# Optimization experiments

Measured on AMD Instinct MI355X. Metric: run time of the kernel, lower is better.

The kernel has to match this reference:

```python
import jax, jax.numpy as jnp
import numpy as np

N = 4096          # num_nodes
E = 65536         # num edges (avg degree 16)
WALK_LENGTH = 16
OUT_DIM = 8


def setup_inputs() -> dict:
    key = jax.random.key(0)
    k1, k2 = jax.random.split(key, 2)
    edge_index = jax.random.randint(k1, (2, E), 0, N, dtype=jnp.int64)
    # nn.Linear(walk_length, out_dim): weight [out_dim, walk_length], bias [out_dim]
    linear_w = (jax.random.normal(k2, (OUT_DIM, WALK_LENGTH), jnp.float32)
                / np.float32(np.sqrt(WALK_LENGTH)))
    linear_b = jnp.zeros((OUT_DIM,), jnp.float32)
    return {"edge_index": edge_index, "num_nodes": N,
            "linear_w": linear_w, "linear_b": linear_b}


def reference(edge_index, num_nodes, linear_w, linear_b):
    row, col = edge_index[0], edge_index[1]
    # out-degree via scatter_add, clamped to >= 1
    deg = jnp.zeros((num_nodes,), jnp.float32).at[row].add(1.0)
    deg = jnp.maximum(deg, 1.0)
    rw_values = 1.0 / deg[row]                              # [E]
    # random-walk transition matrix P[row, col] = 1/deg[row]
    # (.at[].add sums duplicate edges, matching coalesce())
    P = jnp.zeros((num_nodes, num_nodes), jnp.float32).at[row, col].add(rw_values)
    Pt = P.T

    def step(cur, _):
        cur = Pt @ cur                                      # [N, N]
        return cur, jnp.diagonal(cur)                       # k-step return probs

    cur0 = jnp.eye(num_nodes, dtype=jnp.float32)
    _, diags = jax.lax.scan(step, cur0, None, length=WALK_LENGTH)
    rw_diag = diags.T                                       # [N, walk_length]
    return rw_diag @ linear_w.T + linear_b                  # [N, out_dim]
```

## Files before the change

### kernel.cpp

```cpp
#include <hip/hip_runtime.h>
#include <hip/hip_fp16.h>
#include <hip/hip_fp8.h>

#define NNODES 4096
#define LWALK 16
#define ODIM 8

#define FP8_SCALE 256.0f
#define FP8_INV   0.00390625f
#define FP8_INV2  1.52587890625e-05f

typedef unsigned int uint4n __attribute__((ext_vector_type(4)));
typedef float float2n __attribute__((ext_vector_type(2)));

__device__ __forceinline__ void dec8f(unsigned int lo, unsigned int hi, float* f) {
#if __has_builtin(__builtin_amdgcn_cvt_pk_f32_fp8)
    float2n p;
    p = __builtin_amdgcn_cvt_pk_f32_fp8((int)lo, false); f[0] = p.x; f[1] = p.y;
    p = __builtin_amdgcn_cvt_pk_f32_fp8((int)lo, true);  f[2] = p.x; f[3] = p.y;
    p = __builtin_amdgcn_cvt_pk_f32_fp8((int)hi, false); f[4] = p.x; f[5] = p.y;
    p = __builtin_amdgcn_cvt_pk_f32_fp8((int)hi, true);  f[6] = p.x; f[7] = p.y;
#else
    unsigned int w[2] = {lo, hi};
    const unsigned char* b = (const unsigned char*)w;
#pragma unroll
    for (int i = 0; i < 8; ++i) {
        __hip_fp8_e4m3 t; t.__x = b[i]; f[i] = (float)t;
    }
#endif
}

__device__ __forceinline__ void enc8f(const float* a, unsigned int* lo,
                                      unsigned int* hi) {
#if __has_builtin(__builtin_amdgcn_cvt_pk_fp8_f32)
    int l = 0, h = 0;
    l = __builtin_amdgcn_cvt_pk_fp8_f32(a[0], a[1], l, false);
    l = __builtin_amdgcn_cvt_pk_fp8_f32(a[2], a[3], l, true);
    h = __builtin_amdgcn_cvt_pk_fp8_f32(a[4], a[5], h, false);
    h = __builtin_amdgcn_cvt_pk_fp8_f32(a[6], a[7], h, true);
    *lo = (unsigned int)l; *hi = (unsigned int)h;
#else
    unsigned char b[8];
#pragma unroll
    for (int i = 0; i < 8; ++i)
        b[i] = __hip_cvt_float_to_fp8(a[i], __HIP_SATFINITE, __HIP_E4M3);
    unsigned int w[2];
    __builtin_memcpy(w, b, 8);
    *lo = w[0]; *hi = w[1];
#endif
}

__device__ __forceinline__ void dec16f(uint4n w, float* f) {
    dec8f(w.x, w.y, f);
    dec8f(w.z, w.w, f + 8);
}

__device__ __forceinline__ uint4n enc16f(const float* a) {
    uint4n o;
    unsigned int lo, hi;
    enc8f(a, &lo, &hi);     o.x = lo; o.y = hi;
    enc8f(a + 8, &lo, &hi); o.z = lo; o.w = hi;
    return o;
}

__device__ __forceinline__ unsigned char enc1f(float f) {
#if __has_builtin(__builtin_amdgcn_cvt_pk_fp8_f32)
    return (unsigned char)(__builtin_amdgcn_cvt_pk_fp8_f32(f, 0.f, 0, false) & 0xFF);
#else
    return __hip_cvt_float_to_fp8(f, __HIP_SATFINITE, __HIP_E4M3);
#endif
}

__device__ __forceinline__ float decw(unsigned int packed) {
    return __half2float(__ushort_as_half((unsigned short)(packed >> 16)));
}

__global__ void detect_fmt_k(const void* ei, int E, int* flag) {
    if (blockIdx.x == 0 && threadIdx.x == 0) {
        const long long* p = (const long long*)ei;
        int ok = 1;
        for (int i = 0; i < 64; ++i) {
            long long v = p[i];
            if (v < 0 || v >= NNODES) { ok = 0; break; }
        }
        *flag = ok;
    }
}

__device__ __forceinline__ int load_idx(const void* p, int i, int fmt) {
    if (fmt) return (int)((const long long*)p)[i];
    return ((const int*)p)[i];
}

__global__ void build_deg_cnt_k(const void* ei, int E, int* deg, int* cnt,
                                const int* fmt) {
    int e = blockIdx.x * blockDim.x + threadIdx.x;
    if (e >= E) return;
    int f = *fmt;
    int r = load_idx(ei, e, f);
    int c = load_idx(ei, E + e, f);
    atomicAdd(&deg[r], 1);
    atomicAdd(&cnt[c], 1);
}

__global__ void scan_k(const int* __restrict__ cnt, int* __restrict__ rowptr,
                       int* __restrict__ cursor) {
    __shared__ int sm[1024];
    int tid = threadIdx.x;
    int v0 = (cnt[4 * tid + 0] + 3) & ~3;
    int v1 = (cnt[4 * tid + 1] + 3) & ~3;
    int v2 = (cnt[4 * tid + 2] + 3) & ~3;
    int v3 = (cnt[4 * tid + 3] + 3) & ~3;
    int tsum = v0 + v1 + v2 + v3;
    sm[tid] = tsum;
    __syncthreads();
    int val = tsum;
    for (int off = 1; off < 1024; off <<= 1) {
        int t = (tid >= off) ? sm[tid - off] : 0;
        __syncthreads();
        val += t;
        sm[tid] = val;
        __syncthreads();
    }
    int excl = val - tsum;
    int p0 = excl, p1 = excl + v0, p2 = p1 + v1, p3 = p2 + v2;
    rowptr[4 * tid + 0] = p0; rowptr[4 * tid + 1] = p1;
    rowptr[4 * tid + 2] = p2; rowptr[4 * tid + 3] = p3;
    cursor[4 * tid + 0] = p0; cursor[4 * tid + 1] = p1;
    cursor[4 * tid + 2] = p2; cursor[4 * tid + 3] = p3;
    if (tid == 1023) rowptr[4096] = val;
}

__global__ void fill_pad_k(const void* ei, int E, const int* __restrict__ deg,
                           int* cursor, int* ocursor,
                           unsigned int* __restrict__ ep4,
                           unsigned int* __restrict__ oidx, const int* fmt) {
    int e = blockIdx.x * blockDim.x + threadIdx.x;
    if (e < E) {
        int f = *fmt;
        int r = load_idx(ei, e, f);
        int c = load_idx(ei, E + e, f);
        int d = deg[r];
        float v = 1.0f / (float)(d < 1 ? 1 : d);
        int pos = atomicAdd(&cursor[c], 1);
        unsigned hv = (unsigned)__half_as_ushort(__float2half(v));
        ep4[pos] = (hv << 16) | (unsigned)r;
        int opos = atomicAdd(&ocursor[r], 1);
        oidx[opos] = (unsigned)c;
    }
}

__global__ void pad_fill_k(const int* __restrict__ rowptr,
                           const int* __restrict__ cursor,
                           unsigned int* __restrict__ ep4) {
    int c = blockIdx.x * blockDim.x + threadIdx.x;
    if (c >= NNODES) return;
    for (int p = cursor[c]; p < rowptr[c + 1]; ++p)
        ep4[p] = 0u;
}

__global__ __launch_bounds__(512, 1) void chain_k(
    const int* __restrict__ rowptr, const unsigned int* __restrict__ ep4,
    const int* __restrict__ orowptr, const int* __restrict__ ocursor,
    const unsigned int* __restrict__ oidx, const int* __restrict__ deg,
    float* __restrict__ rw,
    unsigned char* __restrict__ M4, unsigned char* __restrict__ M5,
    unsigned char* __restrict__ M7, unsigned char* __restrict__ M8) {
    __shared__ unsigned char bufA[NNODES * 16];
    __shared__ unsigned char bufB[NNODES * 16];
    const int t = threadIdx.x;
    const int bid = blockIdx.x;
    const int slab = (bid & 7) * 32 + (bid >> 3);
    const int S0 = slab * 16;

    float* col32 = (float*)bufB;
    const int g = t >> 4;
    const int l = t & 15;
    for (int cl = 0; cl < 16; ++cl) {
        const int gc = S0 + cl;
        for (int i = t; i < NNODES; i += 512) col32[i] = 0.f;
        __syncthreads();
        const int dg = deg[gc];
        const float vg = 1.f / (float)(dg < 1 ? 1 : dg);
        const int ob = orowptr[gc], oe = ocursor[gc];
        for (int p1 = ob + g; p1 < oe; p1 += 32) {
            int m = (int)oidx[p1];
            if (m == gc && l == 0)
                atomicAdd(&rw[gc * LWALK + 0], vg);
            int dm = deg[m];
            float vm = vg / (float)(dm < 1 ? 1 : dm);
            int mb = orowptr[m], me = ocursor[m];
            for (int p2 = mb + l; p2 < me; p2 += 16)
                atomicAdd(&col32[oidx[p2]], vm);
        }
        __syncthreads();
        if (t == 0) rw[gc * LWALK + 1] = col32[gc];
        for (int i = t; i < NNODES; i += 512)
            bufA[i * 16 + cl] = enc1f(col32[i] * FP8_SCALE);
        __syncthreads();
    }

    int rpb[8], rpe[8];
#pragma unroll
    for (int j = 0; j < 8; ++j) {
        rpb[j] = rowptr[t + 512 * j];
        rpe[j] = rowptr[t + 512 * j + 1];
    }
#pragma unroll 1
    for (int k = 3; k <= 8; ++k) {
        const unsigned char* src = (k & 1) ? bufA : bufB;
        unsigned char* dst = (k & 1) ? bufB : bufA;
        __syncthreads();
#pragma unroll 1
        for (int j = 0; j < 8; ++j) {
            const int c = t + 512 * j;
            float acc[16];
#pragma unroll
            for (int u = 0; u < 16; ++u) acc[u] = 0.f;
            for (int e = rpb[j]; e < rpe[j]; e += 4) {
                uint4n ew = *(const uint4n*)(ep4 + e);
                uint4n x0 = *(const uint4n*)(src + (ew.x & 0xFFFFu) * 16);
                uint4n x1 = *(const uint4n*)(src + (ew.y & 0xFFFFu) * 16);
                uint4n x2 = *(const uint4n*)(src + (ew.z & 0xFFFFu) * 16);
                uint4n x3 = *(const uint4n*)(src + (ew.w & 0xFFFFu) * 16);
                float f[16];
                float v;
                v = decw(ew.x);
                dec16f(x0, f);
#pragma unroll
                for (int u = 0; u < 16; ++u) acc[u] = fmaf(f[u], v, acc[u]);
                v = decw(ew.y);
                dec16f(x1, f);
#pragma unroll
                for (int u = 0; u < 16; ++u) acc[u] = fmaf(f[u], v, acc[u]);
                v = decw(ew.z);
                dec16f(x2, f);
#pragma unroll
                for (int u = 0; u < 16; ++u) acc[u] = fmaf(f[u], v, acc[u]);
                v = decw(ew.w);
                dec16f(x3, f);
#pragma unroll
                for (int u = 0; u < 16; ++u) acc[u] = fmaf(f[u], v, acc[u]);
            }
            if ((unsigned)(c - S0) < 16u) {
                float d = 0.f;
#pragma unroll
                for (int u = 0; u < 16; ++u)
                    if (c - S0 == u) d = acc[u];
                rw[c * LWALK + (k - 1)] = d * FP8_INV;
            }
            uint4n o = enc16f(acc);
            *(uint4n*)(dst + c * 16) = o;
        }
        __syncthreads();
        if (k == 4 || k == 5 || k == 7 || k == 8) {
            unsigned char* M = (k == 4) ? M4 : (k == 5) ? M5 : (k == 7) ? M7 : M8;
#pragma unroll 1
            for (int j = 0; j < 8; ++j) {
                const int c = t + 512 * j;
                uint4n o = *(const uint4n*)(dst + c * 16);
                *(uint4n*)(M + (size_t)c * NNODES + S0) = o;
            }
        }
    }
}

__global__ __launch_bounds__(256) void pairall_k(
    const unsigned char* __restrict__ M4, const unsigned char* __restrict__ M5,
    const unsigned char* __restrict__ M7, const unsigned char* __restrict__ M8,
    float* __restrict__ rw) {
    __shared__ __half bt[64][66];
    __shared__ __half ct[64][66];
    const int bid = blockIdx.x;
    const int grp = bid >> 10;
    const int pb = bid & 1023;
    const unsigned char* PA;
    const unsigned char* PB1;
    const unsigned char* PB2;
    int colO, colE;
    if (grp == 0)      { PA = M5; PB1 = M4; PB2 = M5; colO = 8;  colE = 9;  }
    else if (grp == 1) { PA = M7; PB1 = M4; PB2 = M7; colO = 10; colE = 13; }
    else if (grp == 2) { PA = M8; PB1 = M4; PB2 = M8; colO = 11; colE = 15; }
    else               { PA = M8; PB1 = M5; PB2 = M7; colO = 12; colE = 14; }
    const int i0 = (pb & 63) * 64;
    const int Jbeg = (pb >> 6) * (NNODES / 16);
    const int Jend = Jbeg + (NNODES / 16);
    const int t = threadIdx.x;
    const int li = t >> 2;
    const int q = t & 3;
    const int c0 = q * 16;
    float accO = 0.f, accE = 0.f;
    for (int J = Jbeg; J < Jend; J += 64) {
        uint4n b16 = __builtin_nontemporal_load(
            (const uint4n*)(PB1 + (size_t)(J + li) * NNODES + i0 + c0));
        uint4n g16 = __builtin_nontemporal_load(
            (const uint4n*)(PB2 + (size_t)(J + li) * NNODES + i0 + c0));
        __syncthreads();
        float bf[16], gf[16];
        dec16f(b16, bf);
        dec16f(g16, gf);
#pragma unroll
        for (int s = 0; s < 16; ++s) {
            bt[c0 + s][li] = __float2half(bf[s]);
            ct[c0 + s][li] = __float2half(gf[s]);
        }
        __syncthreads();
        uint4n a16 = __builtin_nontemporal_load(
            (const uint4n*)(PA + (size_t)(i0 + li) * NNODES + J + c0));
        float af[16];
        dec16f(a16, af);
#pragma unroll
        for (int s = 0; s < 16; ++s) {
            accO = fmaf(af[s], __half2float(bt[li][c0 + s]), accO);
            accE = fmaf(af[s], __half2float(ct[li][c0 + s]), accE);
        }
    }
    accO += __shfl_xor(accO, 1);
    accO += __shfl_xor(accO, 2);
    accE += __shfl_xor(accE, 1);
    accE += __shfl_xor(accE, 2);
    if (q == 0) {
        atomicAdd(&rw[(i0 + li) * LWALK + colO], accO * FP8_INV2);
        atomicAdd(&rw[(i0 + li) * LWALK + colE], accE * FP8_INV2);
    }
}

__global__ void linear_k(const float* __restrict__ rw, const float* __restrict__ W,
                         const float* __restrict__ b, float* __restrict__ out) {
    int i = blockIdx.x * blockDim.x + threadIdx.x;
    if (i >= NNODES * ODIM) return;
    int s = i >> 3, d = i & 7;
    float acc = b[d];
#pragma unroll
    for (int k = 0; k < LWALK; ++k)
        acc = fmaf(rw[s * LWALK + k], W[d * LWALK + k], acc);
    out[i] = acc;
}

extern "C" void kernel_launch(void* const* d_in, const int* in_sizes, int n_in,
                              void* d_out, int out_size, void* d_ws, size_t ws_size,
                              hipStream_t stream) {
    const void* ei = d_in[0];
    int E = in_sizes[0] / 2;
    const float* W = (const float*)d_in[2];
    const float* bias = (const float*)d_in[3];
    float* out = (float*)d_out;

    char* ws = (char*)d_ws;
    size_t off = 0;
    auto alloc = [&](size_t bytes) -> char* {
        char* p = ws + off;
        off = (off + bytes + 255) & ~(size_t)255;
        return p;
    };
    int* flag = (int*)alloc(4);
    int* deg = (int*)alloc(NNODES * 4);
    int* cnt = (int*)alloc(NNODES * 4);
    int* rowptr = (int*)alloc((NNODES + 1) * 4);
    int* cursor = (int*)alloc(NNODES * 4);
    int* orowptr = (int*)alloc((NNODES + 1) * 4);
    int* ocursor = (int*)alloc(NNODES * 4);
    unsigned int* ep4 = (unsigned int*)alloc(((size_t)E + 4 * NNODES) * 4);
    unsigned int* oidx = (unsigned int*)alloc(((size_t)E + 4 * NNODES) * 4);
    float* rw = (float*)alloc(NNODES * LWALK * 4);
    unsigned char* M4 = (unsigned char*)alloc((size_t)NNODES * NNODES);
    unsigned char* M5 = (unsigned char*)alloc((size_t)NNODES * NNODES);
    unsigned char* M7 = (unsigned char*)alloc((size_t)NNODES * NNODES);
    unsigned char* M8 = (unsigned char*)alloc((size_t)NNODES * NNODES);

    (void)hipMemsetAsync(deg, 0, NNODES * 4, stream);
    (void)hipMemsetAsync(cnt, 0, NNODES * 4, stream);
    (void)hipMemsetAsync(rw, 0, NNODES * LWALK * 4, stream);
    detect_fmt_k<<<1, 64, 0, stream>>>(ei, E, flag);
    build_deg_cnt_k<<<(E + 255) / 256, 256, 0, stream>>>(ei, E, deg, cnt, flag);
    scan_k<<<1, 1024, 0, stream>>>(cnt, rowptr, cursor);
    scan_k<<<1, 1024, 0, stream>>>(deg, orowptr, ocursor);
    fill_pad_k<<<(E + 255) / 256, 256, 0, stream>>>(ei, E, deg, cursor, ocursor,
                                                    ep4, oidx, flag);
    pad_fill_k<<<(NNODES + 255) / 256, 256, 0, stream>>>(rowptr, cursor, ep4);

    chain_k<<<256, 512, 0, stream>>>(rowptr, ep4, orowptr, ocursor, oidx, deg,
                                     rw, M4, M5, M7, M8);

    pairall_k<<<4096, 256, 0, stream>>>(M4, M5, M7, M8, rw);

    linear_k<<<(NNODES * ODIM + 255) / 256, 256, 0, stream>>>(rw, W, bias, out);
}
```

Measured before the change: 357.9 us.

## Halve chain slab width to 8 columns and launch 512 blocks

The propagation kernel now processes 8 identity columns per block instead of 16, using 32 KiB of LDS per 8-column buffer pair instead of 64 KiB. It launches 512 blocks rather than 256, and the launch bound is raised to allow several blocks per CU. This is meant to raise occupancy and fill more CUs on a 256-CU part. In exchange, the edge list and index loads are repeated twice as often per column, with narrower 8-byte LDS gathers.

```diff
diff --git a/kernel.cpp b/kernel.cpp
--- a/kernel.cpp
+++ b/kernel.cpp
@@ -159,24 +159,23 @@
         ep4[p] = 0u;
 }
 
-__global__ __launch_bounds__(512, 1) void chain_k(
+__global__ __launch_bounds__(512, 4) void chain_k(
     const int* __restrict__ rowptr, const unsigned int* __restrict__ ep4,
     const int* __restrict__ orowptr, const int* __restrict__ ocursor,
     const unsigned int* __restrict__ oidx, const int* __restrict__ deg,
     float* __restrict__ rw,
     unsigned char* __restrict__ M4, unsigned char* __restrict__ M5,
     unsigned char* __restrict__ M7, unsigned char* __restrict__ M8) {
-    __shared__ unsigned char bufA[NNODES * 16];
-    __shared__ unsigned char bufB[NNODES * 16];
+    __shared__ unsigned char buf[2][NNODES * 8];
     const int t = threadIdx.x;
     const int bid = blockIdx.x;
-    const int slab = (bid & 7) * 32 + (bid >> 3);
-    const int S0 = slab * 16;
-
-    float* col32 = (float*)bufB;
+    const int slab = (bid & 7) * 64 + (bid >> 3);
+    const int S0 = slab * 8;
+
+    float* col32 = (float*)buf[1];
     const int g = t >> 4;
     const int l = t & 15;
-    for (int cl = 0; cl < 16; ++cl) {
+    for (int cl = 0; cl < 8; ++cl) {
         const int gc = S0 + cl;
         for (int i = t; i < NNODES; i += 512) col32[i] = 0.f;
         __syncthreads();
@@ -196,7 +195,7 @@
         __syncthreads();
         if (t == 0) rw[gc * LWALK + 1] = col32[gc];
         for (int i = t; i < NNODES; i += 512)
-            bufA[i * 16 + cl] = enc1f(col32[i] * FP8_SCALE);
+            buf[0][i * 8 + cl] = enc1f(col32[i] * FP8_SCALE);
         __syncthreads();
     }
 
@@ -208,49 +207,50 @@
     }
 #pragma unroll 1
     for (int k = 3; k <= 8; ++k) {
-        const unsigned char* src = (k & 1) ? bufA : bufB;
-        unsigned char* dst = (k & 1) ? bufB : bufA;
+        const int si = (k & 1) ^ 1;
+        const int di = k & 1;
         __syncthreads();
 #pragma unroll 1
         for (int j = 0; j < 8; ++j) {
             const int c = t + 512 * j;
-            float acc[16];
-#pragma unroll
-            for (int u = 0; u < 16; ++u) acc[u] = 0.f;
+            float acc[8];
+#pragma unroll
+            for (int u = 0; u < 8; ++u) acc[u] = 0.f;
             for (int e = rpb[j]; e < rpe[j]; e += 4) {
                 uint4n ew = *(const uint4n*)(ep4 + e);
-                uint4n x0 = *(const uint4n*)(src + (ew.x & 0xFFFFu) * 16);
-                uint4n x1 = *(const uint4n*)(src + (ew.y & 0xFFFFu) * 16);
-                uint4n x2 = *(const uint4n*)(src + (ew.z & 0xFFFFu) * 16);
-                uint4n x3 = *(const uint4n*)(src + (ew.w & 0xFFFFu) * 16);
-                float f[16];
+                uint2 x0 = *(const uint2*)&buf[si][(ew.x & 0xFFFFu) * 8];
+                uint2 x1 = *(const uint2*)&buf[si][(ew.y & 0xFFFFu) * 8];
+                uint2 x2 = *(const uint2*)&buf[si][(ew.z & 0xFFFFu) * 8];
+                uint2 x3 = *(const uint2*)&buf[si][(ew.w & 0xFFFFu) * 8];
+                float f[8];
                 float v;
                 v = decw(ew.x);
-                dec16f(x0, f);
-#pragma unroll
-                for (int u = 0; u < 16; ++u) acc[u] = fmaf(f[u], v, acc[u]);
+                dec8f(x0.x, x0.y, f);
+#pragma unroll
+                for (int u = 0; u < 8; ++u) acc[u] = fmaf(f[u], v, acc[u]);
                 v = decw(ew.y);
-                dec16f(x1, f);
-#pragma unroll
-                for (int u = 0; u < 16; ++u) acc[u] = fmaf(f[u], v, acc[u]);
+                dec8f(x1.x, x1.y, f);
+#pragma unroll
+                for (int u = 0; u < 8; ++u) acc[u] = fmaf(f[u], v, acc[u]);
                 v = decw(ew.z);
-                dec16f(x2, f);
-#pragma unroll
-                for (int u = 0; u < 16; ++u) acc[u] = fmaf(f[u], v, acc[u]);
+                dec8f(x2.x, x2.y, f);
+#pragma unroll
+                for (int u = 0; u < 8; ++u) acc[u] = fmaf(f[u], v, acc[u]);
                 v = decw(ew.w);
-                dec16f(x3, f);
-#pragma unroll
-                for (int u = 0; u < 16; ++u) acc[u] = fmaf(f[u], v, acc[u]);
+                dec8f(x3.x, x3.y, f);
+#pragma unroll
+                for (int u = 0; u < 8; ++u) acc[u] = fmaf(f[u], v, acc[u]);
             }
-            if ((unsigned)(c - S0) < 16u) {
+            if ((unsigned)(c - S0) < 8u) {
                 float d = 0.f;
 #pragma unroll
-                for (int u = 0; u < 16; ++u)
+                for (int u = 0; u < 8; ++u)
                     if (c - S0 == u) d = acc[u];
                 rw[c * LWALK + (k - 1)] = d * FP8_INV;
             }
-            uint4n o = enc16f(acc);
-            *(uint4n*)(dst + c * 16) = o;
+            unsigned int lo, hi;
+            enc8f(acc, &lo, &hi);
+            *(uint2*)&buf[di][c * 8] = make_uint2(lo, hi);
         }
         __syncthreads();
         if (k == 4 || k == 5 || k == 7 || k == 8) {
@@ -258,8 +258,8 @@
 #pragma unroll 1
             for (int j = 0; j < 8; ++j) {
                 const int c = t + 512 * j;
-                uint4n o = *(const uint4n*)(dst + c * 16);
-                *(uint4n*)(M + (size_t)c * NNODES + S0) = o;
+                uint2 o = *(const uint2*)&buf[di][c * 8];
+                *(uint2*)(M + (size_t)c * NNODES + S0) = o;
             }
         }
     }
@@ -379,7 +379,7 @@
                                                     ep4, oidx, flag);
     pad_fill_k<<<(NNODES + 255) / 256, 256, 0, stream>>>(rowptr, cursor, ep4);
 
-    chain_k<<<256, 512, 0, stream>>>(rowptr, ep4, orowptr, ocursor, oidx, deg,
+    chain_k<<<512, 512, 0, stream>>>(rowptr, ep4, orowptr, ocursor, oidx, deg,
                                      rw, M4, M5, M7, M8);
 
     pairall_k<<<4096, 256, 0, stream>>>(M4, M5, M7, M8, rw);
```

Measured after the change: 372.4 us. +4.1%, slower.
